# Kernel tuning notes

Measured on AMD Instinct MI355X. Metric: run time of the kernel, lower is better.

The kernel has to match this reference:

```python
import jax, jax.numpy as jnp
import numpy as np

B, S, D, H, E, K = 4, 2048, 768, 3072, 8, 2
CAP_FACTOR = 1.5


def setup_inputs() -> dict:
    key = jax.random.key(0)
    ks = jax.random.split(key, 6)
    x = jax.random.normal(ks[0], (B, S, D), jnp.float32)
    Wr = jax.random.normal(ks[1], (D, E), jnp.float32) * 0.01  # router, std=0.01 init
    w1 = jax.random.normal(ks[2], (E, D, H), jnp.float32) * (1.0 / np.sqrt(D))
    b1 = jnp.zeros((E, H), jnp.float32)
    w2 = jax.random.normal(ks[3], (E, H, D), jnp.float32) * (1.0 / np.sqrt(H))
    b2 = jnp.zeros((E, D), jnp.float32)
    return {"x": x, "Wr": Wr, "w1": w1, "b1": b1, "w2": w2, "b2": b2}


def _moe_forward(x, Wr, w1, b1, w2, b2):
    Bz, Sz, Dz = x.shape
    Ez = Wr.shape[1]
    capacity = int((Bz * Sz / Ez) * CAP_FACTOR)  # 1536

    # --- Router (eval mode: no jitter, no dropout) ---
    logits = x @ Wr                                # [B,S,E]
    probs = jax.nn.softmax(logits, axis=-1)
    topk_p, topk_i = jax.lax.top_k(probs, K)       # [B,S,K]
    topk_p = topk_p / topk_p.sum(-1, keepdims=True)

    # --- Capacity-limited assignment, vectorized equivalent of the serial
    #     (b, s, i) loop: an entry is kept iff fewer than `capacity` earlier
    #     entries (in flat (b,s,i) order) chose the same expert. ---
    e_flat = topk_i.reshape(-1)                    # [N], N = B*S*K, i innermost
    p_flat = topk_p.reshape(-1)
    onehot = (e_flat[:, None] == jnp.arange(Ez)[None, :]).astype(x.dtype)  # [N,E]
    counts_before = jnp.cumsum(onehot, axis=0) - onehot                     # [N,E]
    pos = jnp.take_along_axis(counts_before, e_flat[:, None], axis=1)[:, 0]
    keep = (pos < capacity).astype(x.dtype)        # [N]

    # combine weight per (token, expert): sum over the k slots
    cw = (onehot * (p_flat * keep)[:, None]).reshape(Bz, Sz, K, Ez).sum(2)  # [B,S,E]

    # --- Expert FFNs (dense: every expert on every token, weighted combine) ---
    hidden = jax.nn.gelu(jnp.einsum('bsd,edh->bseh', x, w1) + b1, approximate=False)
    expert_out = jnp.einsum('bseh,ehd->bsed', hidden, w2) + b2               # [B,S,E,D]
    return jnp.einsum('bse,bsed->bsd', cw, expert_out)


def reference(x, Wr, w1, b1, w2, b2):
    return _moe_forward(x, Wr, w1, b1, w2, b2)
```

## Files before the change

### kernel.cpp

```cpp
#include <hip/hip_runtime.h>
#include <hip/hip_bf16.h>
#include <math.h>

#define TOK    8192
#define DMODEL 768
#define HDIM   3072
#define NEXP   8
#define CAP    1536
#define NFLAT  (TOK*2)

typedef __attribute__((ext_vector_type(8))) short bf16x8;
typedef __attribute__((ext_vector_type(4))) float f32x4;

static __device__ __forceinline__ unsigned short f2bf(float f) {
  unsigned int u = __float_as_uint(f);
  u += 0x7FFF + ((u >> 16) & 1);
  return (unsigned short)(u >> 16);
}

static __device__ __forceinline__ float fast_gelu(float v) {
  const float v2 = v * v;
  const float y2 = v * (1.59576912f + 0.07135534f * v2);
  const float e  = __expf(y2);
  return v - v * __builtin_amdgcn_rcpf(e + 1.0f);
}

__global__ __launch_bounds__(256)
void moe_router(const float* __restrict__ x, const float* __restrict__ Wr,
                int* __restrict__ eidx, float* __restrict__ pw)
{
  const int wid = threadIdx.x >> 6, lane = threadIdx.x & 63;
  const int t = blockIdx.x * 4 + wid;
  const float* xr = x + (size_t)t * DMODEL;
  double acc[NEXP];
#pragma unroll
  for (int e = 0; e < NEXP; ++e) acc[e] = 0.0;
  for (int j = 0; j < DMODEL / 64; ++j) {
    const int d = j * 64 + lane;
    const double xv = (double)xr[d];
    const float* wrow = Wr + (size_t)d * NEXP;
#pragma unroll
    for (int e = 0; e < NEXP; ++e) acc[e] += xv * (double)wrow[e];
  }
#pragma unroll
  for (int off = 32; off > 0; off >>= 1) {
#pragma unroll
    for (int e = 0; e < NEXP; ++e) acc[e] += __shfl_xor(acc[e], off, 64);
  }
  if (lane == 0) {
    int e0 = 0;
    for (int e = 1; e < NEXP; ++e) if (acc[e] > acc[e0]) e0 = e;
    int e1 = (e0 == 0) ? 1 : 0;
    for (int e = 0; e < NEXP; ++e) { if (e == e0) continue; if (acc[e] > acc[e1]) e1 = e; }
    const double p0 = 1.0 / (1.0 + exp(acc[e1] - acc[e0]));
    eidx[t * 2 + 0] = e0; eidx[t * 2 + 1] = e1;
    pw[t * 2 + 0] = (float)p0; pw[t * 2 + 1] = (float)(1.0 - p0);
  }
}

__global__ __launch_bounds__(256)
void moe_assign(const int* __restrict__ eidx, int* __restrict__ slotpos,
                int* __restrict__ elist, int* __restrict__ counts)
{
  const int e = blockIdx.x;
  const int tid = threadIdx.x;
  const int base = tid * 64;
  const int4* p4 = (const int4*)(eidx + base);
  int cnt = 0;
#pragma unroll
  for (int j = 0; j < 16; ++j) {
    int4 v = p4[j];
    cnt += (v.x == e) + (v.y == e) + (v.z == e) + (v.w == e);
  }
  const int lane = tid & 63, wid = tid >> 6;
  int incl = cnt;
  for (int off = 1; off < 64; off <<= 1) {
    int u = __shfl_up(incl, off, 64);
    if (lane >= off) incl += u;
  }
  __shared__ int wsum[4];
  if (lane == 63) wsum[wid] = incl;
  __syncthreads();
  int wbase = 0;
  for (int w = 0; w < wid; ++w) wbase += wsum[w];
  int run = wbase + incl - cnt;
#pragma unroll
  for (int j = 0; j < 16; ++j) {
    int4 v = p4[j];
    const int n = base + j * 4;
    int vv[4] = {v.x, v.y, v.z, v.w};
#pragma unroll
    for (int q = 0; q < 4; ++q) {
      if (vv[q] == e) {
        const int pos = run++;
        slotpos[n + q] = (pos < CAP) ? pos : -1;
        if (pos < CAP) elist[e * CAP + pos] = (n + q) >> 1;
      }
    }
  }
  if (tid == 255) {
    int tot = wbase + incl;
    counts[e] = (tot < CAP) ? tot : CAP;
  }
}

__global__ __launch_bounds__(256)
void transpose_bf16(const float* __restrict__ in, unsigned short* __restrict__ out,
                    int R, int C)
{
  __shared__ unsigned short tile[64][65];
  const int e = blockIdx.z;
  in  += (size_t)e * R * C;
  out += (size_t)e * C * R;
  const int c0 = blockIdx.x * 64, r0 = blockIdx.y * 64;
  const int tid = threadIdx.x;
  const int rL = tid >> 4;
  const int cq = (tid & 15) * 4;
#pragma unroll
  for (int p = 0; p < 4; ++p) {
    const int r = rL + p * 16;
    float4 v = *(const float4*)&in[(size_t)(r0 + r) * C + c0 + cq];
    tile[r][cq + 0] = f2bf(v.x);
    tile[r][cq + 1] = f2bf(v.y);
    tile[r][cq + 2] = f2bf(v.z);
    tile[r][cq + 3] = f2bf(v.w);
  }
  __syncthreads();
  const int cL = tid >> 4;
  const int rq = (tid & 15) * 4;
#pragma unroll
  for (int p = 0; p < 4; ++p) {
    const int cc = cL + p * 16;
    ushort4 o;
    o.x = tile[rq + 0][cc]; o.y = tile[rq + 1][cc];
    o.z = tile[rq + 2][cc]; o.w = tile[rq + 3][cc];
    *(ushort4*)&out[(size_t)(c0 + cc) * R + r0 + rq] = o;
  }
}

__global__ __launch_bounds__(64)
void moe_gather(const float* __restrict__ x, const int* __restrict__ elist,
                const int* __restrict__ counts, unsigned short* __restrict__ Xg)
{
  const int p = blockIdx.x, e = blockIdx.y;
  const int lane = threadIdx.x;
  unsigned short* dst = Xg + ((size_t)e * CAP + p) * DMODEL;
  if (p >= counts[e]) {
    ushort4 z; z.x = z.y = z.z = z.w = 0;
#pragma unroll
    for (int j = 0; j < 3; ++j) ((ushort4*)dst)[j * 64 + lane] = z;
    return;
  }
  const int tok = elist[e * CAP + p];
  const float4* src = (const float4*)(x + (size_t)tok * DMODEL);
#pragma unroll
  for (int j = 0; j < 3; ++j) {
    float4 v = src[j * 64 + lane];
    ushort4 o;
    o.x = f2bf(v.x); o.y = f2bf(v.y); o.z = f2bf(v.z); o.w = f2bf(v.w);
    ((ushort4*)dst)[j * 64 + lane] = o;
  }
}

template <int EPI, int ORD>
__global__ __launch_bounds__(256)
void moe_rs(const unsigned short* __restrict__ Ag, int lda,
            const unsigned short* __restrict__ Bg, int ldb,
            void* __restrict__ Cout0, void* __restrict__ Cout1, int ldc,
            const float* __restrict__ bias,
            int Nsize, int NT, int MT, int NTN)
{
  __shared__ __align__(16) unsigned short lds[2 * 8192];
  unsigned short* const ldsA = lds;
  unsigned short* const ldsB = lds + 8192;

  const int cpx = gridDim.x >> 3;
  const int swz = (blockIdx.x & 7) * cpx + (blockIdx.x >> 3);
  const int e  = swz / cpx;
  int rd = swz - e * cpx;
  int mt, nt, ks;
  if (ORD == 0) { mt = rd % MT;  rd /= MT;  nt = rd % NTN; ks = rd / NTN; }
  else          { nt = rd % NTN; rd /= NTN; mt = rd % MT;  ks = rd / MT;  }
  const int m0 = mt * 128, n0 = nt * 128;
  const int kb = ks * NT * 64;

  const unsigned short* Ae = Ag + (size_t)e * CAP * lda;
  const unsigned short* Be = Bg + (size_t)e * Nsize * ldb;

  const int tid = threadIdx.x, lane = tid & 63, wid = tid >> 6;
  const int wr = wid >> 1, wc = wid & 1;
  const int r16 = lane & 15, g4 = lane >> 4;

  const int srow  = tid >> 3;
  const int scol  = tid & 7;
  const int scolX = scol ^ (srow & 7);
  const unsigned short* pA = Ae + (size_t)(m0 + srow) * lda + scol * 8 + kb;
  const unsigned short* pB = Be + (size_t)(n0 + srow) * ldb + scol * 8 + kb;
  unsigned short* qA = &ldsA[srow * 64 + scolX * 8];
  unsigned short* qB = &ldsB[srow * 64 + scolX * 8];

  float4 a0, a1, a2, a3, b0, b1, b2, b3;

#define LOADT(tt) do {                                                        \
    const size_t ko = (size_t)(tt) * 64;                                      \
    a0 = *(const float4*)(pA + ko);                                           \
    a1 = *(const float4*)(pA + ko + (size_t)32 * lda);                        \
    a2 = *(const float4*)(pA + ko + (size_t)64 * lda);                        \
    a3 = *(const float4*)(pA + ko + (size_t)96 * lda);                        \
    b0 = *(const float4*)(pB + ko);                                           \
    b1 = *(const float4*)(pB + ko + (size_t)32 * ldb);                        \
    b2 = *(const float4*)(pB + ko + (size_t)64 * ldb);                        \
    b3 = *(const float4*)(pB + ko + (size_t)96 * ldb);                        \
  } while (0)

#define STORET() do {                                                         \
    *(float4*)(qA)        = a0;  *(float4*)(qA + 2048) = a1;                  \
    *(float4*)(qA + 4096) = a2;  *(float4*)(qA + 6144) = a3;                  \
    *(float4*)(qB)        = b0;  *(float4*)(qB + 2048) = b1;                  \
    *(float4*)(qB + 4096) = b2;  *(float4*)(qB + 6144) = b3;                  \
  } while (0)

  f32x4 acc[4][4];
#pragma unroll
  for (int i = 0; i < 4; ++i)
#pragma unroll
    for (int j = 0; j < 4; ++j) acc[i][j] = (f32x4){0.f, 0.f, 0.f, 0.f};

  const int cx0 = (g4 ^ (r16 & 7)) * 8;
  const int rA = (wr * 64 + r16) * 64;
  const int rB = (wc * 64 + r16) * 64;

  LOADT(0);
  for (int t = 0; t < NT; ++t) {
    __syncthreads();
    STORET();
    if (t + 1 < NT) LOADT(t + 1);
    __syncthreads();
#pragma unroll
    for (int kh = 0; kh < 2; ++kh) {
      const int cx = cx0 ^ (kh * 32);
      bf16x8 aF[4], bF[4];
#pragma unroll
      for (int mi = 0; mi < 4; ++mi)
        aF[mi] = *(const bf16x8*)&ldsA[rA + mi * 1024 + cx];
#pragma unroll
      for (int ni = 0; ni < 4; ++ni)
        bF[ni] = *(const bf16x8*)&ldsB[rB + ni * 1024 + cx];
#pragma unroll
      for (int mi = 0; mi < 4; ++mi)
#pragma unroll
        for (int ni = 0; ni < 4; ++ni)
          acc[mi][ni] = __builtin_amdgcn_mfma_f32_16x16x32_bf16(aF[mi], bF[ni], acc[mi][ni], 0, 0, 0);
    }
  }
#undef LOADT
#undef STORET

  const float* bvec = bias + (size_t)e * Nsize;
  if constexpr (EPI == 0) {
    __syncthreads();
#pragma unroll
    for (int ni = 0; ni < 4; ++ni) {
      const int lc = wc * 64 + ni * 16 + r16;
      const float bv = bvec[n0 + lc];
#pragma unroll
      for (int mi = 0; mi < 4; ++mi) {
        const int lr0 = wr * 64 + mi * 16 + 4 * g4;
#pragma unroll
        for (int reg = 0; reg < 4; ++reg) {
          lds[(lr0 + reg) * 128 + lc] = f2bf(fast_gelu(acc[mi][ni][reg] + bv));
        }
      }
    }
    __syncthreads();
    unsigned short* C = (unsigned short*)Cout0 + (size_t)e * CAP * ldc;
#pragma unroll
    for (int it = 0; it < 8; ++it) {
      const int chunk = it * 256 + tid;
      const int row = chunk >> 4, c8 = chunk & 15;
      *(float4*)(C + (size_t)(m0 + row) * ldc + n0 + c8 * 8) = *(const float4*)&lds[chunk * 8];
    }
  } else {
    float* C = (float*)(ks ? Cout1 : Cout0) + (size_t)e * CAP * ldc;
#pragma unroll
    for (int ni = 0; ni < 4; ++ni) {
      const int gc = n0 + wc * 64 + ni * 16 + r16;
#pragma unroll
      for (int mi = 0; mi < 4; ++mi) {
        const int gr0 = m0 + wr * 64 + mi * 16 + 4 * g4;
#pragma unroll
        for (int reg = 0; reg < 4; ++reg)
          C[(size_t)(gr0 + reg) * ldc + gc] = acc[mi][ni][reg];
      }
    }
  }
}

__global__ __launch_bounds__(192)
void moe_combine(const float* __restrict__ Y0, const float* __restrict__ Y1,
                 const float* __restrict__ b2, const int* __restrict__ eidx,
                 const float* __restrict__ pw, const int* __restrict__ slotpos,
                 float* __restrict__ out)
{
  const int t = blockIdx.x;
  const int tid = threadIdx.x;
  float4 acc; acc.x = acc.y = acc.z = acc.w = 0.f;
#pragma unroll
  for (int s = 0; s < 2; ++s) {
    const int pos = slotpos[t * 2 + s];
    if (pos >= 0) {
      const int e = eidx[t * 2 + s];
      const float w = pw[t * 2 + s];
      const size_t ro = ((size_t)e * CAP + pos) * DMODEL;
      float4 y0 = ((const float4*)(Y0 + ro))[tid];
      float4 y1 = ((const float4*)(Y1 + ro))[tid];
      float4 bv = ((const float4*)(b2 + (size_t)e * DMODEL))[tid];
      acc.x += w * (y0.x + y1.x + bv.x);
      acc.y += w * (y0.y + y1.y + bv.y);
      acc.z += w * (y0.z + y1.z + bv.z);
      acc.w += w * (y0.w + y1.w + bv.w);
    }
  }
  ((float4*)out)[(size_t)t * (DMODEL / 4) + tid] = acc;
}

extern "C" void kernel_launch(void* const* d_in, const int* in_sizes, int n_in,
                              void* d_out, int out_size, void* d_ws, size_t ws_size,
                              hipStream_t stream)
{
  const float* x  = (const float*)d_in[0];
  const float* Wr = (const float*)d_in[1];
  const float* w1 = (const float*)d_in[2];
  const float* b1 = (const float*)d_in[3];
  const float* w2 = (const float*)d_in[4];
  const float* b2 = (const float*)d_in[5];
  float* out = (float*)d_out;

  char* ws = (char*)d_ws;
  const size_t SZ_W1T = (size_t)NEXP * HDIM * DMODEL * 2;
  const size_t SZ_W2T = (size_t)NEXP * DMODEL * HDIM * 2;
  const size_t SZ_XG  = (size_t)NEXP * CAP * DMODEL * 2;
  const size_t SZ_H   = (size_t)NEXP * CAP * HDIM * 2;
  const size_t SZ_Y   = (size_t)NEXP * CAP * DMODEL * 4;
  unsigned short* w1t = (unsigned short*)(ws);               size_t off = SZ_W1T;
  unsigned short* w2t = (unsigned short*)(ws + off);         off += SZ_W2T;
  unsigned short* Xg  = (unsigned short*)(ws + off);         off += SZ_XG;
  unsigned short* Hb  = (unsigned short*)(ws + off);         off += SZ_H;
  float*          Y0  = (float*)(ws + off);                  off += SZ_Y;
  int*   eidx    = (int*)(ws + off);                         off += (size_t)TOK * 2 * 4;
  float* pw      = (float*)(ws + off);                       off += (size_t)TOK * 2 * 4;
  int*   slotpos = (int*)(ws + off);                         off += (size_t)NFLAT * 4;
  int*   elist   = (int*)(ws + off);                         off += (size_t)NEXP * CAP * 4;
  int*   counts  = (int*)(ws + off);
  float* Y1 = (float*)w1t;

  moe_router<<<TOK / 4, 256, 0, stream>>>(x, Wr, eidx, pw);
  moe_assign<<<NEXP, 256, 0, stream>>>(eidx, slotpos, elist, counts);
  transpose_bf16<<<dim3(HDIM / 64, DMODEL / 64, NEXP), 256, 0, stream>>>(w1, w1t, DMODEL, HDIM);
  transpose_bf16<<<dim3(DMODEL / 64, HDIM / 64, NEXP), 256, 0, stream>>>(w2, w2t, HDIM, DMODEL);
  moe_gather<<<dim3(CAP, NEXP), 64, 0, stream>>>(x, elist, counts, Xg);
  moe_rs<0, 0><<<2304, 256, 0, stream>>>(
      Xg, DMODEL, w1t, DMODEL, Hb, Hb, HDIM, b1, HDIM, 12, 12, 24);
  moe_rs<1, 1><<<1152, 256, 0, stream>>>(
      Hb, HDIM, w2t, HDIM, Y0, Y1, DMODEL, b2, DMODEL, 24, 12, 6);
  moe_combine<<<TOK, 192, 0, stream>>>(Y0, Y1, b2, eidx, pw, slotpos, out);
}
```

Baseline: 237.7 us.

## Use 256x128 tiles with a dedicated kernel for the first expert GEMM

Adds a specialized GEMM kernel for the up-projection with GELU epilogue that computes 256x128 output tiles per block (8x4 MFMA fragments per wave) instead of the previous smaller tiles. The grid is halved, to 1152 blocks. Each loaded B tile is now reused across twice as many rows, which cuts global and LDS traffic per MFMA. The cost is higher register pressure from the 128 accumulator floats plus 12 staged float4 loads, a larger LDS footprint, and fewer blocks, which could lower occupancy.

```diff
diff --git a/kernel.cpp b/kernel.cpp
--- a/kernel.cpp
+++ b/kernel.cpp
@@ -159,6 +159,133 @@
     ushort4 o;
     o.x = f2bf(v.x); o.y = f2bf(v.y); o.z = f2bf(v.z); o.w = f2bf(v.w);
     ((ushort4*)dst)[j * 64 + lane] = o;
+  }
+}
+
+__global__ __launch_bounds__(256)
+void moe_rs8(const unsigned short* __restrict__ Ag, int lda,
+             const unsigned short* __restrict__ Bg, int ldb,
+             unsigned short* __restrict__ Cout, int ldc,
+             const float* __restrict__ bias,
+             int Nsize, int NT, int MT, int NTN)
+{
+  __shared__ __align__(16) unsigned short lds[16384 + 8192];
+  unsigned short* const ldsA = lds;
+  unsigned short* const ldsB = lds + 16384;
+
+  const int cpx = gridDim.x >> 3;
+  const int swz = (blockIdx.x & 7) * cpx + (blockIdx.x >> 3);
+  const int e  = swz / cpx;
+  int rd = swz - e * cpx;
+  const int mt = rd % MT;
+  const int nt = rd / MT;
+  const int m0 = mt * 256, n0 = nt * 128;
+
+  const unsigned short* Ae = Ag + (size_t)e * CAP * lda;
+  const unsigned short* Be = Bg + (size_t)e * Nsize * ldb;
+
+  const int tid = threadIdx.x, lane = tid & 63, wid = tid >> 6;
+  const int wr = wid >> 1, wc = wid & 1;
+  const int r16 = lane & 15, g4 = lane >> 4;
+
+  const int srow  = tid >> 3;
+  const int scol  = tid & 7;
+  const int scolX = scol ^ (srow & 7);
+  const unsigned short* pA = Ae + (size_t)(m0 + srow) * lda + scol * 8;
+  const unsigned short* pB = Be + (size_t)(n0 + srow) * ldb + scol * 8;
+  unsigned short* qA = &ldsA[srow * 64 + scolX * 8];
+  unsigned short* qB = &ldsB[srow * 64 + scolX * 8];
+
+  float4 a0, a1, a2, a3, a4, a5, a6, a7, b0, b1, b2, b3;
+
+#define LOADT(tt) do {                                                        \
+    const size_t ko = (size_t)(tt) * 64;                                      \
+    a0 = *(const float4*)(pA + ko);                                           \
+    a1 = *(const float4*)(pA + ko + (size_t)32  * lda);                       \
+    a2 = *(const float4*)(pA + ko + (size_t)64  * lda);                       \
+    a3 = *(const float4*)(pA + ko + (size_t)96  * lda);                       \
+    a4 = *(const float4*)(pA + ko + (size_t)128 * lda);                       \
+    a5 = *(const float4*)(pA + ko + (size_t)160 * lda);                       \
+    a6 = *(const float4*)(pA + ko + (size_t)192 * lda);                       \
+    a7 = *(const float4*)(pA + ko + (size_t)224 * lda);                       \
+    b0 = *(const float4*)(pB + ko);                                           \
+    b1 = *(const float4*)(pB + ko + (size_t)32  * ldb);                       \
+    b2 = *(const float4*)(pB + ko + (size_t)64  * ldb);                       \
+    b3 = *(const float4*)(pB + ko + (size_t)96  * ldb);                       \
+  } while (0)
+
+#define STORET() do {                                                         \
+    *(float4*)(qA)         = a0;  *(float4*)(qA + 2048)  = a1;                \
+    *(float4*)(qA + 4096)  = a2;  *(float4*)(qA + 6144)  = a3;                \
+    *(float4*)(qA + 8192)  = a4;  *(float4*)(qA + 10240) = a5;                \
+    *(float4*)(qA + 12288) = a6;  *(float4*)(qA + 14336) = a7;                \
+    *(float4*)(qB)         = b0;  *(float4*)(qB + 2048)  = b1;                \
+    *(float4*)(qB + 4096)  = b2;  *(float4*)(qB + 6144)  = b3;                \
+  } while (0)
+
+  f32x4 acc[8][4];
+#pragma unroll
+  for (int i = 0; i < 8; ++i)
+#pragma unroll
+    for (int j = 0; j < 4; ++j) acc[i][j] = (f32x4){0.f, 0.f, 0.f, 0.f};
+
+  const int cx0 = (g4 ^ (r16 & 7)) * 8;
+  const int rA = (wr * 128 + r16) * 64;
+  const int rB = (wc * 64 + r16) * 64;
+
+  LOADT(0);
+  for (int t = 0; t < NT; ++t) {
+    __syncthreads();
+    STORET();
+    if (t + 1 < NT) LOADT(t + 1);
+    __syncthreads();
+#pragma unroll
+    for (int kh = 0; kh < 2; ++kh) {
+      const int cx = cx0 ^ (kh * 32);
+      bf16x8 aF[8], bF[4];
+#pragma unroll
+      for (int mi = 0; mi < 8; ++mi)
+        aF[mi] = *(const bf16x8*)&ldsA[rA + mi * 1024 + cx];
+#pragma unroll
+      for (int ni = 0; ni < 4; ++ni)
+        bF[ni] = *(const bf16x8*)&ldsB[rB + ni * 1024 + cx];
+#pragma unroll
+      for (int mi = 0; mi < 8; ++mi)
+#pragma unroll
+        for (int ni = 0; ni < 4; ++ni)
+          acc[mi][ni] = __builtin_amdgcn_mfma_f32_16x16x32_bf16(aF[mi], bF[ni], acc[mi][ni], 0, 0, 0);
+    }
+  }
+#undef LOADT
+#undef STORET
+
+  const float* bvec = bias + (size_t)e * Nsize;
+#pragma unroll
+  for (int p = 0; p < 2; ++p) {
+    __syncthreads();
+    if (wr == p) {
+#pragma unroll
+      for (int ni = 0; ni < 4; ++ni) {
+        const int lc = wc * 64 + ni * 16 + r16;
+        const float bv = bvec[n0 + lc];
+#pragma unroll
+        for (int mi = 0; mi < 8; ++mi) {
+          const int lr0 = mi * 16 + 4 * g4;
+#pragma unroll
+          for (int reg = 0; reg < 4; ++reg)
+            lds[(lr0 + reg) * 128 + lc] = f2bf(fast_gelu(acc[mi][ni][reg] + bv));
+        }
+      }
+    }
+    __syncthreads();
+    unsigned short* C = Cout + (size_t)e * CAP * ldc;
+#pragma unroll
+    for (int it = 0; it < 8; ++it) {
+      const int chunk = it * 256 + tid;
+      const int row = chunk >> 4, c8 = chunk & 15;
+      *(float4*)(C + (size_t)(m0 + p * 128 + row) * ldc + n0 + c8 * 8) =
+          *(const float4*)&lds[chunk * 8];
+    }
   }
 }
 
@@ -359,8 +486,8 @@
   transpose_bf16<<<dim3(HDIM / 64, DMODEL / 64, NEXP), 256, 0, stream>>>(w1, w1t, DMODEL, HDIM);
   transpose_bf16<<<dim3(DMODEL / 64, HDIM / 64, NEXP), 256, 0, stream>>>(w2, w2t, HDIM, DMODEL);
   moe_gather<<<dim3(CAP, NEXP), 64, 0, stream>>>(x, elist, counts, Xg);
-  moe_rs<0, 0><<<2304, 256, 0, stream>>>(
-      Xg, DMODEL, w1t, DMODEL, Hb, Hb, HDIM, b1, HDIM, 12, 12, 24);
+  moe_rs8<<<1152, 256, 0, stream>>>(
+      Xg, DMODEL, w1t, DMODEL, Hb, HDIM, b1, HDIM, 12, 6, 24);
   moe_rs<1, 1><<<1152, 256, 0, stream>>>(
       Hb, HDIM, w2t, HDIM, Y0, Y1, DMODEL, b2, DMODEL, 24, 12, 6);
   moe_combine<<<TOK, 192, 0, stream>>>(Y0, Y1, b2, eidx, pw, slotpos, out);
```

Result: slower. 292.9 us (+23.2%).
